# Performance work log

Measured on AMD Instinct MI355X. Metric: run time of the kernel, lower is better.

Reference implementation:

```python
import jax, jax.numpy as jnp
import numpy as np

B, S, D = 2, 4096, 768
H = 12
HD = D // H  # 64


def setup_inputs() -> dict:
    key = jax.random.key(0)
    ks = jax.random.split(key, 5)
    scale = 1.0 / np.sqrt(D)
    x = jax.random.normal(ks[0], (B, S, D), dtype=jnp.float32)
    Wq = jax.random.normal(ks[1], (D, D), dtype=jnp.float32) * scale
    Wk = jax.random.normal(ks[2], (D, D), dtype=jnp.float32) * scale
    Wv = jax.random.normal(ks[3], (D, D), dtype=jnp.float32) * scale
    Wo = jax.random.normal(ks[4], (D, D), dtype=jnp.float32) * scale
    zb = jnp.zeros((D,), dtype=jnp.float32)
    return {"x": x, "Wq": Wq, "bq": zb, "Wk": Wk, "bk": zb, "Wv": Wv, "bv": zb, "Wo": Wo, "bo": zb}


def reference(x, Wq, bq, Wk, bk, Wv, bv, Wo, bo):
    b, s, d = x.shape
    # projections: nn.Linear computes x @ W^T + b; here W is stored as [in, out]-style [D, D]
    def proj(W, bias):
        y = jnp.einsum('bsd,ed->bse', x, W) + bias  # matches torch Linear (weight [out,in])
        return y.reshape(b, s, H, HD).transpose(0, 2, 1, 3)  # [B,H,S,HD]
    q = proj(Wq, bq)
    k = proj(Wk, bk)
    v = proj(Wv, bv)
    att = jnp.einsum('bhqd,bhkd->bhqk', q, k) / np.sqrt(HD).astype(np.float32)
    causal = jnp.tril(jnp.ones((s, s), dtype=bool))
    att = jnp.where(causal, att, -jnp.inf)
    att = jax.nn.softmax(att, axis=-1)  # dropout p=0 (eval)
    y = jnp.einsum('bhqk,bhkd->bhqd', att, v)
    y = y.transpose(0, 2, 1, 3).reshape(b, s, d)
    return jnp.einsum('bsd,ed->bse', y, Wo) + bo
```

## Files before the change

kernel.cpp:

```cpp
#include <hip/hip_runtime.h>
#include <hip/hip_bf16.h>

typedef __bf16 bf16;
typedef __attribute__((ext_vector_type(8))) __bf16 bf16x8;
typedef __attribute__((ext_vector_type(4))) __bf16 bf16x4;
typedef __attribute__((ext_vector_type(4))) float f32x4;
typedef __attribute__((ext_vector_type(16))) float f32x16;

#if __has_builtin(__builtin_amdgcn_permlane32_swap)
#define HAVE_PLSWAP 1
typedef __attribute__((ext_vector_type(2))) unsigned uint2v;
#endif

#define MFMA16(a, b, c) __builtin_amdgcn_mfma_f32_16x16x32_bf16((a), (b), (c), 0, 0, 0)
#define MFMA32(a, b, c) __builtin_amdgcn_mfma_f32_32x32x16_bf16((a), (b), (c), 0, 0, 0)

__device__ __forceinline__ void gload_lds16(const bf16* g, bf16* l) {
  __builtin_amdgcn_global_load_lds(
      (const __attribute__((address_space(1))) void*)g,
      (__attribute__((address_space(3))) void*)l, 16, 0, 0);
}

__device__ __forceinline__ unsigned pkbf(float a, float b) {
  union { unsigned u; bf16 h[2]; } w;
  w.h[0] = (bf16)a; w.h[1] = (bf16)b;
  return w.u;
}

#define CBAR(N)                                               \
  do {                                                        \
    asm volatile("s_waitcnt vmcnt(" #N ") lgkmcnt(0)" ::: "memory"); \
    __builtin_amdgcn_s_barrier();                             \
    __builtin_amdgcn_sched_barrier(0);                        \
  } while (0)

__global__ void cvt_all(const float* __restrict__ x,
                        const float* __restrict__ wq, const float* __restrict__ wk,
                        const float* __restrict__ wv, const float* __restrict__ wo,
                        bf16* __restrict__ xb, bf16* __restrict__ Wb) {
  constexpr int NX4 = 6291456 / 4;
  constexpr int NW4 = 589824 / 4;
  constexpr int TOT = NX4 + 4 * NW4;
  int stride = gridDim.x * blockDim.x;
  for (int i = blockIdx.x * blockDim.x + threadIdx.x; i < TOT; i += stride) {
    const float4* src;
    bf16x4* dst;
    if (i < NX4) {
      src = reinterpret_cast<const float4*>(x) + i;
      dst = reinterpret_cast<bf16x4*>(xb) + i;
    } else {
      int j = i - NX4;
      int w = j / NW4, r = j - w * NW4;
      const float* sp = (w == 0) ? wq : (w == 1) ? wk : (w == 2) ? wv : wo;
      src = reinterpret_cast<const float4*>(sp) + r;
      dst = reinterpret_cast<bf16x4*>(Wb) + j;
    }
    float4 v = *src;
    bf16x4 o = {(bf16)v.x, (bf16)v.y, (bf16)v.z, (bf16)v.w};
    *dst = o;
  }
}

template <bool OUT_BF16, int BN>
__global__ __launch_bounds__(256) void gemm_bt(
    const bf16* __restrict__ A, const bf16* __restrict__ W,
    const float* __restrict__ b0, const float* __restrict__ b1, const float* __restrict__ b2,
    float* __restrict__ Cf, bf16* __restrict__ Cb,
    int M, int N, int K) {
  const int total = gridDim.x * gridDim.y * gridDim.z;
  const int nb = total >> 3;
  const int lin = blockIdx.x + gridDim.x * (blockIdx.y + gridDim.y * blockIdx.z);
  const int virt = (lin & 7) * nb + (lin >> 3);
  const int bx = virt % gridDim.x;
  const int rest = virt / gridDim.x;
  const int by = rest % gridDim.y;
  const int z = rest / gridDim.y;

  const bf16* Wz = W + (size_t)z * N * K;
  const float* bias = (z == 0) ? b0 : (z == 1 ? b1 : b2);
  const float oscale = (OUT_BF16 && z == 0) ? 0.125f * 1.44269504089f : 1.0f;

  constexpr int NFR = BN / 64;
  __shared__ alignas(16) bf16 As[128 * 64];
  __shared__ alignas(16) bf16 Bs[BN * 64];

  const int tid = threadIdx.x;
  const int wave = tid >> 6, lane = tid & 63;
  const int lr = lane & 15, lg = lane >> 4;
  const int wr = wave >> 1, wc = wave & 1;
  const int m0 = by * 128, n0 = bx * BN;

  f32x4 acc[4][2 * NFR] = {};

  for (int k0 = 0; k0 < K; k0 += 64) {
    __syncthreads();
#pragma unroll
    for (int j = 0; j < 4; ++j) {
      int cb = j * 256 + wave * 64;
      int c = cb + tid - wave * 64 + wave * 64;
      c = cb + lane;
      int row = c >> 3, x = c & 7;
      int xs = x ^ (row & 7);
      gload_lds16(&A[(size_t)(m0 + row) * K + k0 + xs * 8], &As[cb * 8]);
    }
#pragma unroll
    for (int j = 0; j < BN / 32; ++j) {
      int cb = j * 256 + wave * 64;
      int c = cb + lane;
      int row = c >> 3, x = c & 7;
      int xs = x ^ (row & 7);
      gload_lds16(&Wz[(size_t)(n0 + row) * K + k0 + xs * 8], &Bs[cb * 8]);
    }
    __syncthreads();
#pragma unroll
    for (int kk = 0; kk < 2; ++kk) {
      bf16x8 af[4], bfr[2 * NFR];
#pragma unroll
      for (int m = 0; m < 4; ++m) {
        int row = wr * 64 + m * 16 + lr;
        int ch = (kk * 4 + lg) ^ (row & 7);
        af[m] = *reinterpret_cast<const bf16x8*>(&As[row * 64 + ch * 8]);
      }
#pragma unroll
      for (int n = 0; n < 2 * NFR; ++n) {
        int row = wc * (BN / 2) + n * 16 + lr;
        int ch = (kk * 4 + lg) ^ (row & 7);
        bfr[n] = *reinterpret_cast<const bf16x8*>(&Bs[row * 64 + ch * 8]);
      }
      __builtin_amdgcn_s_setprio(1);
#pragma unroll
      for (int m = 0; m < 4; ++m)
#pragma unroll
        for (int n = 0; n < 2 * NFR; ++n)
          acc[m][n] = MFMA16(af[m], bfr[n], acc[m][n]);
      __builtin_amdgcn_s_setprio(0);
    }
  }

#pragma unroll
  for (int m = 0; m < 4; ++m) {
#pragma unroll
    for (int n = 0; n < 2 * NFR; ++n) {
#pragma unroll
      for (int i = 0; i < 4; ++i) {
        int row = m0 + wr * 64 + m * 16 + lg * 4 + i;
        int col = n0 + wc * (BN / 2) + n * 16 + lr;
        float v = (acc[m][n][i] + bias[col]) * oscale;
        if constexpr (OUT_BF16)
          (Cb + (size_t)z * M * N)[(size_t)row * N + col] = (bf16)v;
        else
          Cf[(size_t)row * N + col] = v;
      }
    }
  }
}

__global__ __launch_bounds__(256, 3) void attn32(
    const bf16* __restrict__ Q, const bf16* __restrict__ K,
    const bf16* __restrict__ V, bf16* __restrict__ Y) {
  constexpr int S = 4096, D = 768;
  const int lin = blockIdx.x;
  const int xcd = lin & 7, idx = lin >> 3;
  const int seg = idx >> 5;
  const int pair = xcd * 3 + seg;
  const int jj = idx & 31;
  const int qb = (seg == 0) ? jj
               : (seg == 1) ? ((jj + 16) & 31)
               : (jj < 16 ? 30 - 2 * jj : 63 - 2 * jj);
  const int h = pair % 12, bb = pair / 12;

  const int tid = threadIdx.x, wave = tid >> 6, lane = tid & 63;
  const int ln = lane & 31, hi = lane >> 5;

  const int qw0 = qb * 128 + wave * 32;
  const int qrow = qw0 + ln;
  const int nt = 2 * qb + 2;

  __shared__ alignas(16) bf16 Ks[3][64 * 64];
  __shared__ alignas(16) bf16 Vt[2][64 * 64];

  const size_t head = (size_t)bb * S * D + (size_t)h * 64;

  union U32x4 { unsigned u[4]; bf16x8 v; };
  U32x4 onesU;
  onesU.u[0] = onesU.u[1] = onesU.u[2] = onesU.u[3] = 0x3F803F80u;
  const bf16x8 onesf = onesU.v;

  const f32x16 z16 = {};

  bf16x8 qf[4];
  {
    const bf16* qp = Q + head + (size_t)qrow * D;
#pragma unroll
    for (int c = 0; c < 4; ++c)
      qf[c] = *reinterpret_cast<const bf16x8*>(qp + c * 16 + hi * 8);
  }

  int fOff[4];
#pragma unroll
  for (int i = 0; i < 4; ++i)
    fOff[i] = ln * 64 + ((((2 * i + hi) ^ ln) & 7) * 8);

  const bf16* gk[2];
  int ldsK[2];
#pragma unroll
  for (int j2 = 0; j2 < 2; ++j2) {
    int c = j2 * 256 + tid;
    int r = c >> 3, ch = c & 7;
    gk[j2] = K + head + (size_t)r * D + ((ch ^ (r & 7)) & 7) * 8;
    ldsK[j2] = (j2 * 256 + wave * 64) * 8;
  }

  const int k0v = (tid & 31) * 2, d0 = (tid >> 5) * 8;
  const bf16* gv0 = V + head + (size_t)k0v * D + d0;
  const bf16* gv1 = gv0 + D;
  int wOff[8];
#pragma unroll
  for (int e = 0; e < 8; ++e)
    wOff[e] = (d0 + e) * 64 + ((((k0v >> 3) ^ e) & 7) * 8) + (k0v & 7);

  f32x16 accO0 = {}, accO1 = {}, accL = {};

  auto stageK = [&](int buf) {
#pragma unroll
    for (int j2 = 0; j2 < 2; ++j2) {
      gload_lds16(gk[j2], &Ks[buf][ldsK[j2]]);
      gk[j2] += 64 * D;
    }
  };
  auto loadV = [&](bf16x8* vv) {
    vv[0] = *reinterpret_cast<const bf16x8*>(gv0);
    vv[1] = *reinterpret_cast<const bf16x8*>(gv1);
    gv0 += 64 * D;
    gv1 += 64 * D;
  };
  auto writeV = [&](const bf16x8* vv, int buf) {
#pragma unroll
    for (int e = 0; e < 8; ++e) {
      union { unsigned u; bf16 h[2]; } pw;
      pw.h[0] = vv[0][e]; pw.h[1] = vv[1][e];
      *reinterpret_cast<unsigned*>(&Vt[buf][wOff[e]]) = pw.u;
    }
  };

  {
    bf16x8 v0[2];
    loadV(v0);
    stageK(0);
    stageK(1);
    writeV(v0, 0);
  }
  CBAR(2);

  int curV = 0, curK = 0, sK = 2;
  for (int t = 0; t < nt; ++t) {
    const int kv0 = t * 64;
    const bool more = (t + 1 < nt);
    bf16x8 vnext[2];
    if (more) {
      loadV(vnext);
      if (t + 2 < nt) { stageK(sK); sK = (sK == 2) ? 0 : sK + 1; }
    }

    if (kv0 <= qw0 + 31) {
      const bf16* ksp = &Ks[curK][0];
      f32x16 s0, s1;
      __builtin_amdgcn_s_setprio(1);
      {
        bf16x8 kf0 = *reinterpret_cast<const bf16x8*>(ksp + fOff[0]);
        bf16x8 kf1 = *reinterpret_cast<const bf16x8*>(ksp + fOff[0] + 2048);
        s0 = MFMA32(kf0, qf[0], z16);
        s1 = MFMA32(kf1, qf[0], z16);
      }
#pragma unroll
      for (int c = 1; c < 4; ++c) {
        bf16x8 kf0 = *reinterpret_cast<const bf16x8*>(ksp + fOff[c]);
        bf16x8 kf1 = *reinterpret_cast<const bf16x8*>(ksp + fOff[c] + 2048);
        s0 = MFMA32(kf0, qf[c], s0);
        s1 = MFMA32(kf1, qf[c], s1);
      }
      __builtin_amdgcn_s_setprio(0);

      if (kv0 + 63 > qw0) {
#pragma unroll
        for (int r = 0; r < 16; ++r) {
          int kl = (r & 3) + 8 * (r >> 2) + 4 * hi;
          if (kv0 + kl > qrow) s0[r] = -1e30f;
          if (kv0 + 32 + kl > qrow) s1[r] = -1e30f;
        }
      }

      float p[32];
#pragma unroll
      for (int r = 0; r < 16; ++r) {
        p[r] = __builtin_amdgcn_exp2f(s0[r]);
        p[16 + r] = __builtin_amdgcn_exp2f(s1[r]);
      }

      const bf16* vtp = &Vt[curV][0];
      __builtin_amdgcn_s_setprio(1);
#pragma unroll
      for (int kg = 0; kg < 2; ++kg) {
        const float* pv = &p[kg * 16];
        unsigned w0 = pkbf(pv[0], pv[1]), w1 = pkbf(pv[2], pv[3]);
        unsigned w2 = pkbf(pv[4], pv[5]), w3 = pkbf(pv[6], pv[7]);
        unsigned w4 = pkbf(pv[8], pv[9]), w5 = pkbf(pv[10], pv[11]);
        unsigned w6 = pkbf(pv[12], pv[13]), w7 = pkbf(pv[14], pv[15]);
        union { unsigned u[4]; bf16x8 v; } fe, fo;
#if HAVE_PLSWAP
        uint2v r02 = __builtin_amdgcn_permlane32_swap(w0, w2, false, false);
        uint2v r13 = __builtin_amdgcn_permlane32_swap(w1, w3, false, false);
        uint2v r46 = __builtin_amdgcn_permlane32_swap(w4, w6, false, false);
        uint2v r57 = __builtin_amdgcn_permlane32_swap(w5, w7, false, false);
        fe.u[0] = r02.x; fe.u[1] = r13.x; fe.u[2] = r02.y; fe.u[3] = r13.y;
        fo.u[0] = r46.x; fo.u[1] = r57.x; fo.u[2] = r46.y; fo.u[3] = r57.y;
#else
        unsigned X0 = hi ? w0 : w2, X1 = hi ? w1 : w3;
        unsigned X2 = hi ? w4 : w6, X3 = hi ? w5 : w7;
        unsigned Y0 = __shfl_xor((int)X0, 32), Y1 = __shfl_xor((int)X1, 32);
        unsigned Y2 = __shfl_xor((int)X2, 32), Y3 = __shfl_xor((int)X3, 32);
        fe.u[0] = hi ? Y0 : w0; fe.u[1] = hi ? Y1 : w1;
        fe.u[2] = hi ? w2 : Y0; fe.u[3] = hi ? w3 : Y1;
        fo.u[0] = hi ? Y2 : w4; fo.u[1] = hi ? Y3 : w5;
        fo.u[2] = hi ? w6 : Y2; fo.u[3] = hi ? w7 : Y3;
#endif
#pragma unroll
        for (int half = 0; half < 2; ++half) {
          int kc = 2 * kg + half;
          bf16x8 pf = half ? fo.v : fe.v;
          bf16x8 vf0 = *reinterpret_cast<const bf16x8*>(vtp + fOff[kc]);
          bf16x8 vf1 = *reinterpret_cast<const bf16x8*>(vtp + fOff[kc] + 2048);
          accO0 = MFMA32(vf0, pf, accO0);
          accO1 = MFMA32(vf1, pf, accO1);
          accL = MFMA32(onesf, pf, accL);
        }
      }
      __builtin_amdgcn_s_setprio(0);
    }

    if (more) {
      writeV(vnext, curV ^ 1);
      CBAR(2);
      curV ^= 1;
      curK = (curK == 2) ? 0 : curK + 1;
    }
  }

  float inv = 1.f / accL[0];
  bf16* yp = Y + head + (size_t)qrow * D;
#pragma unroll
  for (int g = 0; g < 4; ++g) {
    bf16x4 o0, o1;
#pragma unroll
    for (int i = 0; i < 4; ++i) {
      o0[i] = (bf16)(accO0[g * 4 + i] * inv);
      o1[i] = (bf16)(accO1[g * 4 + i] * inv);
    }
    *reinterpret_cast<bf16x4*>(yp + 8 * g + 4 * hi) = o0;
    *reinterpret_cast<bf16x4*>(yp + 32 + 8 * g + 4 * hi) = o1;
  }
}

extern "C" void kernel_launch(void* const* d_in, const int* in_sizes, int n_in,
                              void* d_out, int out_size, void* d_ws, size_t ws_size,
                              hipStream_t stream) {
  const float* x  = (const float*)d_in[0];
  const float* Wq = (const float*)d_in[1];
  const float* bq = (const float*)d_in[2];
  const float* Wk = (const float*)d_in[3];
  const float* bk = (const float*)d_in[4];
  const float* Wv = (const float*)d_in[5];
  const float* bv = (const float*)d_in[6];
  const float* Wo = (const float*)d_in[7];
  const float* bo = (const float*)d_in[8];
  float* out = (float*)d_out;

  constexpr int Bx = 2, S = 4096, Dd = 768;
  constexpr int M = Bx * S;
  constexpr size_t XB = (size_t)M * Dd;
  constexpr size_t WB = (size_t)Dd * Dd;

  char* ws = (char*)d_ws;
  bf16* xb = (bf16*)ws;
  bf16* Wb = (bf16*)(ws + 2 * XB);
  bf16* Qb = (bf16*)(ws + 2 * XB + 8 * WB);
  bf16* Kb = Qb + XB;
  bf16* Vb = Kb + XB;
  bf16* Yb = Vb + XB;

  cvt_all<<<2048, 256, 0, stream>>>(x, Wq, Wk, Wv, Wo, xb, Wb);

  gemm_bt<true, 128><<<dim3(6, 64, 3), 256, 0, stream>>>(
      xb, Wb, bq, bk, bv, nullptr, Qb, M, Dd, Dd);

  attn32<<<dim3(768), 256, 0, stream>>>(Qb, Kb, Vb, Yb);

  gemm_bt<false, 64><<<dim3(12, 64, 1), 256, 0, stream>>>(
      Yb, Wb + 3 * WB, bo, bo, bo, out, nullptr, M, Dd, Dd);
}
```

Before: 170.5 us.

## Process 64 query rows per wave in attention, halving waves per block

The attention kernel now runs 2 waves per block instead of 4. Each wave handles two 32-row query sub-tiles that share every K and V fragment read from LDS, which doubles register-level reuse and cuts LDS fragment reads per query row. K/V staging is redistributed over 128 threads, with wider V transposition writes. The cost is more accumulator registers, lower occupancy (launch bounds 128,2) and fewer waves to hide latency.

```diff
diff --git a/kernel.cpp b/kernel.cpp
--- a/kernel.cpp
+++ b/kernel.cpp
@@ -97,8 +97,7 @@
 #pragma unroll
     for (int j = 0; j < 4; ++j) {
       int cb = j * 256 + wave * 64;
-      int c = cb + tid - wave * 64 + wave * 64;
-      c = cb + lane;
+      int c = cb + lane;
       int row = c >> 3, x = c & 7;
       int xs = x ^ (row & 7);
       gload_lds16(&A[(size_t)(m0 + row) * K + k0 + xs * 8], &As[cb * 8]);
@@ -155,7 +154,7 @@
   }
 }
 
-__global__ __launch_bounds__(256, 3) void attn32(
+__global__ __launch_bounds__(128, 2) void attn32(
     const bf16* __restrict__ Q, const bf16* __restrict__ K,
     const bf16* __restrict__ V, bf16* __restrict__ Y) {
   constexpr int S = 4096, D = 768;
@@ -172,8 +171,9 @@
   const int tid = threadIdx.x, wave = tid >> 6, lane = tid & 63;
   const int ln = lane & 31, hi = lane >> 5;
 
-  const int qw0 = qb * 128 + wave * 32;
-  const int qrow = qw0 + ln;
+  const int qw0 = qb * 128 + wave * 64;
+  const int qrowA = qw0 + ln;
+  const int qrowB = qw0 + 32 + ln;
   const int nt = 2 * qb + 2;
 
   __shared__ alignas(16) bf16 Ks[3][64 * 64];
@@ -188,12 +188,15 @@
 
   const f32x16 z16 = {};
 
-  bf16x8 qf[4];
+  bf16x8 qfA[4], qfB[4];
   {
-    const bf16* qp = Q + head + (size_t)qrow * D;
-#pragma unroll
-    for (int c = 0; c < 4; ++c)
-      qf[c] = *reinterpret_cast<const bf16x8*>(qp + c * 16 + hi * 8);
+    const bf16* qpA = Q + head + (size_t)qrowA * D;
+    const bf16* qpB = Q + head + (size_t)qrowB * D;
+#pragma unroll
+    for (int c = 0; c < 4; ++c) {
+      qfA[c] = *reinterpret_cast<const bf16x8*>(qpA + c * 16 + hi * 8);
+      qfB[c] = *reinterpret_cast<const bf16x8*>(qpB + c * 16 + hi * 8);
+    }
   }
 
   int fOff[4];
@@ -201,83 +204,120 @@
   for (int i = 0; i < 4; ++i)
     fOff[i] = ln * 64 + ((((2 * i + hi) ^ ln) & 7) * 8);
 
-  const bf16* gk[2];
-  int ldsK[2];
-#pragma unroll
-  for (int j2 = 0; j2 < 2; ++j2) {
-    int c = j2 * 256 + tid;
+  const bf16* gk[4];
+  int ldsK[4];
+#pragma unroll
+  for (int j2 = 0; j2 < 4; ++j2) {
+    int c = j2 * 128 + tid;
     int r = c >> 3, ch = c & 7;
     gk[j2] = K + head + (size_t)r * D + ((ch ^ (r & 7)) & 7) * 8;
-    ldsK[j2] = (j2 * 256 + wave * 64) * 8;
-  }
-
-  const int k0v = (tid & 31) * 2, d0 = (tid >> 5) * 8;
-  const bf16* gv0 = V + head + (size_t)k0v * D + d0;
-  const bf16* gv1 = gv0 + D;
+    ldsK[j2] = (j2 * 128 + wave * 64) * 8;
+  }
+
+  const int k0v = (tid & 15) * 4, d0 = (tid >> 4) * 8;
+  const bf16* gv[4];
+#pragma unroll
+  for (int m = 0; m < 4; ++m) gv[m] = V + head + (size_t)(k0v + m) * D + d0;
   int wOff[8];
 #pragma unroll
   for (int e = 0; e < 8; ++e)
     wOff[e] = (d0 + e) * 64 + ((((k0v >> 3) ^ e) & 7) * 8) + (k0v & 7);
 
-  f32x16 accO0 = {}, accO1 = {}, accL = {};
+  f32x16 accOA0 = {}, accOA1 = {}, accOB0 = {}, accOB1 = {};
+  f32x16 accLA = {}, accLB = {};
 
   auto stageK = [&](int buf) {
 #pragma unroll
-    for (int j2 = 0; j2 < 2; ++j2) {
+    for (int j2 = 0; j2 < 4; ++j2) {
       gload_lds16(gk[j2], &Ks[buf][ldsK[j2]]);
       gk[j2] += 64 * D;
     }
   };
   auto loadV = [&](bf16x8* vv) {
-    vv[0] = *reinterpret_cast<const bf16x8*>(gv0);
-    vv[1] = *reinterpret_cast<const bf16x8*>(gv1);
-    gv0 += 64 * D;
-    gv1 += 64 * D;
+#pragma unroll
+    for (int m = 0; m < 4; ++m) {
+      vv[m] = *reinterpret_cast<const bf16x8*>(gv[m]);
+      gv[m] += 64 * D;
+    }
   };
   auto writeV = [&](const bf16x8* vv, int buf) {
 #pragma unroll
     for (int e = 0; e < 8; ++e) {
-      union { unsigned u; bf16 h[2]; } pw;
-      pw.h[0] = vv[0][e]; pw.h[1] = vv[1][e];
-      *reinterpret_cast<unsigned*>(&Vt[buf][wOff[e]]) = pw.u;
+      bf16x4 pw = {vv[0][e], vv[1][e], vv[2][e], vv[3][e]};
+      *reinterpret_cast<bf16x4*>(&Vt[buf][wOff[e]]) = pw;
     }
   };
 
+  auto packP = [&](const float* p, bf16x8* pa) {
+#pragma unroll
+    for (int kg = 0; kg < 2; ++kg) {
+      const float* pv = &p[kg * 16];
+      unsigned w0 = pkbf(pv[0], pv[1]), w1 = pkbf(pv[2], pv[3]);
+      unsigned w2 = pkbf(pv[4], pv[5]), w3 = pkbf(pv[6], pv[7]);
+      unsigned w4 = pkbf(pv[8], pv[9]), w5 = pkbf(pv[10], pv[11]);
+      unsigned w6 = pkbf(pv[12], pv[13]), w7 = pkbf(pv[14], pv[15]);
+      union { unsigned u[4]; bf16x8 v; } fe, fo;
+#if HAVE_PLSWAP
+      uint2v r02 = __builtin_amdgcn_permlane32_swap(w0, w2, false, false);
+      uint2v r13 = __builtin_amdgcn_permlane32_swap(w1, w3, false, false);
+      uint2v r46 = __builtin_amdgcn_permlane32_swap(w4, w6, false, false);
+      uint2v r57 = __builtin_amdgcn_permlane32_swap(w5, w7, false, false);
+      fe.u[0] = r02.x; fe.u[1] = r13.x; fe.u[2] = r02.y; fe.u[3] = r13.y;
+      fo.u[0] = r46.x; fo.u[1] = r57.x; fo.u[2] = r46.y; fo.u[3] = r57.y;
+#else
+      unsigned X0 = hi ? w0 : w2, X1 = hi ? w1 : w3;
+      unsigned X2 = hi ? w4 : w6, X3 = hi ? w5 : w7;
+      unsigned Y0 = __shfl_xor((int)X0, 32), Y1 = __shfl_xor((int)X1, 32);
+      unsigned Y2 = __shfl_xor((int)X2, 32), Y3 = __shfl_xor((int)X3, 32);
+      fe.u[0] = hi ? Y0 : w0; fe.u[1] = hi ? Y1 : w1;
+      fe.u[2] = hi ? w2 : Y0; fe.u[3] = hi ? w3 : Y1;
+      fo.u[0] = hi ? Y2 : w4; fo.u[1] = hi ? Y3 : w5;
+      fo.u[2] = hi ? w6 : Y2; fo.u[3] = hi ? w7 : Y3;
+#endif
+      pa[2 * kg] = fe.v;
+      pa[2 * kg + 1] = fo.v;
+    }
+  };
+
   {
-    bf16x8 v0[2];
+    bf16x8 v0[4];
     loadV(v0);
     stageK(0);
     stageK(1);
     writeV(v0, 0);
   }
-  CBAR(2);
+  CBAR(4);
 
   int curV = 0, curK = 0, sK = 2;
   for (int t = 0; t < nt; ++t) {
     const int kv0 = t * 64;
     const bool more = (t + 1 < nt);
-    bf16x8 vnext[2];
+    bf16x8 vnext[4];
     if (more) {
       loadV(vnext);
       if (t + 2 < nt) { stageK(sK); sK = (sK == 2) ? 0 : sK + 1; }
     }
 
-    if (kv0 <= qw0 + 31) {
+    if (kv0 <= qw0 + 63) {
       const bf16* ksp = &Ks[curK][0];
-      f32x16 s0, s1;
+      f32x16 sA0, sA1, sB0, sB1;
       __builtin_amdgcn_s_setprio(1);
       {
         bf16x8 kf0 = *reinterpret_cast<const bf16x8*>(ksp + fOff[0]);
         bf16x8 kf1 = *reinterpret_cast<const bf16x8*>(ksp + fOff[0] + 2048);
-        s0 = MFMA32(kf0, qf[0], z16);
-        s1 = MFMA32(kf1, qf[0], z16);
+        sA0 = MFMA32(kf0, qfA[0], z16);
+        sA1 = MFMA32(kf1, qfA[0], z16);
+        sB0 = MFMA32(kf0, qfB[0], z16);
+        sB1 = MFMA32(kf1, qfB[0], z16);
       }
 #pragma unroll
       for (int c = 1; c < 4; ++c) {
         bf16x8 kf0 = *reinterpret_cast<const bf16x8*>(ksp + fOff[c]);
         bf16x8 kf1 = *reinterpret_cast<const bf16x8*>(ksp + fOff[c] + 2048);
-        s0 = MFMA32(kf0, qf[c], s0);
-        s1 = MFMA32(kf1, qf[c], s1);
+        sA0 = MFMA32(kf0, qfA[c], sA0);
+        sA1 = MFMA32(kf1, qfA[c], sA1);
+        sB0 = MFMA32(kf0, qfB[c], sB0);
+        sB1 = MFMA32(kf1, qfB[c], sB1);
       }
       __builtin_amdgcn_s_setprio(0);
 
@@ -285,79 +325,85 @@
 #pragma unroll
         for (int r = 0; r < 16; ++r) {
           int kl = (r & 3) + 8 * (r >> 2) + 4 * hi;
-          if (kv0 + kl > qrow) s0[r] = -1e30f;
-          if (kv0 + 32 + kl > qrow) s1[r] = -1e30f;
+          if (kv0 + kl > qrowA) sA0[r] = -1e30f;
+          if (kv0 + 32 + kl > qrowA) sA1[r] = -1e30f;
+          if (kv0 + 32 + kl > qrowB) sB1[r] = -1e30f;
         }
       }
 
-      float p[32];
-#pragma unroll
-      for (int r = 0; r < 16; ++r) {
-        p[r] = __builtin_amdgcn_exp2f(s0[r]);
-        p[16 + r] = __builtin_amdgcn_exp2f(s1[r]);
+      bf16x8 paA[4], paB[4];
+      {
+        float p[32];
+#pragma unroll
+        for (int r = 0; r < 16; ++r) {
+          p[r] = __builtin_amdgcn_exp2f(sA0[r]);
+          p[16 + r] = __builtin_amdgcn_exp2f(sA1[r]);
+        }
+        packP(p, paA);
+      }
+      {
+        float p[32];
+#pragma unroll
+        for (int r = 0; r < 16; ++r) {
+          p[r] = __builtin_amdgcn_exp2f(sB0[r]);
+          p[16 + r] = __builtin_amdgcn_exp2f(sB1[r]);
+        }
+        packP(p, paB);
       }
 
       const bf16* vtp = &Vt[curV][0];
       __builtin_amdgcn_s_setprio(1);
 #pragma unroll
-      for (int kg = 0; kg < 2; ++kg) {
-        const float* pv = &p[kg * 16];
-        unsigned w0 = pkbf(pv[0], pv[1]), w1 = pkbf(pv[2], pv[3]);
-        unsigned w2 = pkbf(pv[4], pv[5]), w3 = pkbf(pv[6], pv[7]);
-        unsigned w4 = pkbf(pv[8], pv[9]), w5 = pkbf(pv[10], pv[11]);
-        unsigned w6 = pkbf(pv[12], pv[13]), w7 = pkbf(pv[14], pv[15]);
-        union { unsigned u[4]; bf16x8 v; } fe, fo;
-#if HAVE_PLSWAP
-        uint2v r02 = __builtin_amdgcn_permlane32_swap(w0, w2, false, false);
-        uint2v r13 = __builtin_amdgcn_permlane32_swap(w1, w3, false, false);
-        uint2v r46 = __builtin_amdgcn_permlane32_swap(w4, w6, false, false);
-        uint2v r57 = __builtin_amdgcn_permlane32_swap(w5, w7, false, false);
-        fe.u[0] = r02.x; fe.u[1] = r13.x; fe.u[2] = r02.y; fe.u[3] = r13.y;
-        fo.u[0] = r46.x; fo.u[1] = r57.x; fo.u[2] = r46.y; fo.u[3] = r57.y;
-#else
-        unsigned X0 = hi ? w0 : w2, X1 = hi ? w1 : w3;
-        unsigned X2 = hi ? w4 : w6, X3 = hi ? w5 : w7;
-        unsigned Y0 = __shfl_xor((int)X0, 32), Y1 = __shfl_xor((int)X1, 32);
-        unsigned Y2 = __shfl_xor((int)X2, 32), Y3 = __shfl_xor((int)X3, 32);
-        fe.u[0] = hi ? Y0 : w0; fe.u[1] = hi ? Y1 : w1;
-        fe.u[2] = hi ? w2 : Y0; fe.u[3] = hi ? w3 : Y1;
-        fo.u[0] = hi ? Y2 : w4; fo.u[1] = hi ? Y3 : w5;
-        fo.u[2] = hi ? w6 : Y2; fo.u[3] = hi ? w7 : Y3;
-#endif
-#pragma unroll
-        for (int half = 0; half < 2; ++half) {
-          int kc = 2 * kg + half;
-          bf16x8 pf = half ? fo.v : fe.v;
-          bf16x8 vf0 = *reinterpret_cast<const bf16x8*>(vtp + fOff[kc]);
-          bf16x8 vf1 = *reinterpret_cast<const bf16x8*>(vtp + fOff[kc] + 2048);
-          accO0 = MFMA32(vf0, pf, accO0);
-          accO1 = MFMA32(vf1, pf, accO1);
-          accL = MFMA32(onesf, pf, accL);
-        }
+      for (int kc = 0; kc < 4; ++kc) {
+        bf16x8 vf0 = *reinterpret_cast<const bf16x8*>(vtp + fOff[kc]);
+        bf16x8 vf1 = *reinterpret_cast<const bf16x8*>(vtp + fOff[kc] + 2048);
+        accOA0 = MFMA32(vf0, paA[kc], accOA0);
+        accOA1 = MFMA32(vf1, paA[kc], accOA1);
+        accLA = MFMA32(onesf, paA[kc], accLA);
+        accOB0 = MFMA32(vf0, paB[kc], accOB0);
+        accOB1 = MFMA32(vf1, paB[kc], accOB1);
+        accLB = MFMA32(onesf, paB[kc], accLB);
       }
       __builtin_amdgcn_s_setprio(0);
     }
 
     if (more) {
       writeV(vnext, curV ^ 1);
-      CBAR(2);
+      CBAR(4);
       curV ^= 1;
       curK = (curK == 2) ? 0 : curK + 1;
     }
   }
 
-  float inv = 1.f / accL[0];
-  bf16* yp = Y + head + (size_t)qrow * D;
-#pragma unroll
-  for (int g = 0; g < 4; ++g) {
-    bf16x4 o0, o1;
-#pragma unroll
-    for (int i = 0; i < 4; ++i) {
-      o0[i] = (bf16)(accO0[g * 4 + i] * inv);
-      o1[i] = (bf16)(accO1[g * 4 + i] * inv);
-    }
-    *reinterpret_cast<bf16x4*>(yp + 8 * g + 4 * hi) = o0;
-    *reinterpret_cast<bf16x4*>(yp + 32 + 8 * g + 4 * hi) = o1;
+  {
+    float inv = 1.f / accLA[0];
+    bf16* yp = Y + head + (size_t)qrowA * D;
+#pragma unroll
+    for (int g = 0; g < 4; ++g) {
+      bf16x4 o0, o1;
+#pragma unroll
+      for (int i = 0; i < 4; ++i) {
+        o0[i] = (bf16)(accOA0[g * 4 + i] * inv);
+        o1[i] = (bf16)(accOA1[g * 4 + i] * inv);
+      }
+      *reinterpret_cast<bf16x4*>(yp + 8 * g + 4 * hi) = o0;
+      *reinterpret_cast<bf16x4*>(yp + 32 + 8 * g + 4 * hi) = o1;
+    }
+  }
+  {
+    float inv = 1.f / accLB[0];
+    bf16* yp = Y + head + (size_t)qrowB * D;
+#pragma unroll
+    for (int g = 0; g < 4; ++g) {
+      bf16x4 o0, o1;
+#pragma unroll
+      for (int i = 0; i < 4; ++i) {
+        o0[i] = (bf16)(accOB0[g * 4 + i] * inv);
+        o1[i] = (bf16)(accOB1[g * 4 + i] * inv);
+      }
+      *reinterpret_cast<bf16x4*>(yp + 8 * g + 4 * hi) = o0;
+      *reinterpret_cast<bf16x4*>(yp + 32 + 8 * g + 4 * hi) = o1;
+    }
   }
 }
 
@@ -393,7 +439,7 @@
   gemm_bt<true, 128><<<dim3(6, 64, 3), 256, 0, stream>>>(
       xb, Wb, bq, bk, bv, nullptr, Qb, M, Dd, Dd);
 
-  attn32<<<dim3(768), 256, 0, stream>>>(Qb, Kb, Vb, Yb);
+  attn32<<<dim3(768), 128, 0, stream>>>(Qb, Kb, Vb, Yb);
 
   gemm_bt<false, 64><<<dim3(12, 64, 1), 256, 0, stream>>>(
       Yb, Wb + 3 * WB, bo, bo, bo, out, nullptr, M, Dd, Dd);
```

New measurement: 210.5 us. +23.5%, slower.
